# Performance work log

Measured on AMD Instinct MI355X. Metric: run time of the kernel, lower is better.

Reference implementation:

```python
import jax, jax.numpy as jnp
import numpy as np
from jax import lax

N_STEPS = 96
N_MAT = 4
N_STRIKES = 201
PERIOD = N_STEPS // N_MAT  # 24
BATCH = 8192
T_HORIZON = 2.0
RFR = 0.05
S0 = 100.0
DT = T_HORIZON / N_STEPS
SQRT_DT = DT ** 0.5
DF = float(np.exp(-RFR * DT))  # one-step discount factor


def _drift_nets(p, x):
    # x: [3, B]; three stacked MLPs (sigma_S, b_V, sigma_V), n=net axis -> [3, 1, B]
    W0, b0, W1, b1, W2, b2, W3, b3 = p
    h = jax.nn.relu(jnp.einsum('nof,fb->nob', W0, x) + b0[:, :, None])
    h = jax.nn.relu(jnp.einsum('nof,nfb->nob', W1, h) + b1[:, :, None])
    h = jax.nn.relu(jnp.einsum('nof,nfb->nob', W2, h) + b2[:, :, None])
    return jnp.einsum('nof,nfb->nob', W3, h) + b3[:, :, None]


def _hedge_net(p, x):
    # x: [2, B] -> [N_STRIKES*N_MAT, B]
    W0, b0, W1, b1, W2, b2, W3, b3, W4, b4 = p
    h = jax.nn.relu(W0 @ x + b0[:, None])
    h = jax.nn.relu(W1 @ h + b1[:, None])
    h = jax.nn.relu(W2 @ h + b2[:, None])
    h = jax.nn.relu(W3 @ h + b3[:, None])
    return W4 @ h + b4[:, None]


def _forward(nW0, nb0, nW1, nb1, nW2, nb2, nW3, nb3,
             hW0, hb0, hW1, hb1, hW2, hb2, hW3, hb3, hW4, hb4,
             rho, V0, strikes, noise1, noise2, remat=False):
    dtype = noise1.dtype
    B = noise1.shape[1]
    rho_s = rho[0]
    S = jnp.full((B,), S0, dtype)
    V = jnp.ones((B,), dtype) * V0[0]
    H = jnp.zeros((N_STRIKES, N_MAT, B), dtype)  # hedging accumulator
    prices = jnp.zeros((N_STRIKES, N_MAT), dtype)
    variance = jnp.zeros((N_STRIKES, N_MAT), dtype)
    for m in range(N_MAT):  # one MLP set per maturity period (timegridNet idx)
        nP = (nW0[:, m], nb0[:, m], nW1[:, m], nb1[:, m],
              nW2[:, m], nb2[:, m], nW3[:, m], nb3[:, m])
        hP = (hW0[m], hb0[m], hW1[m], hb1[m], hW2[m], hb2[m],
              hW3[m], hb3[m], hW4[m], hb4[m])

        def step(carry, xs, nP=nP, hP=hP):
            S, V, H = carry
            t_i, n1, n2 = xs
            t = t_i * jnp.ones_like(S)
            X = jnp.stack([t, S, V], 0)  # [3, B]
            raw = _drift_nets(nP, X)
            raw_d = _drift_nets(nP, lax.stop_gradient(X))  # X.detach() path
            vals = raw / (1.0 + jnp.abs(raw_d) * SQRT_DT)
            sig_S, b_V, sig_V = vals[0, 0], vals[1, 0], vals[2, 0]
            b_S = S * RFR / (1.0 + jnp.abs(lax.stop_gradient(S) * RFR) * SQRT_DT)
            dW = SQRT_DT * n2
            dB = rho_s * dW + jnp.sqrt(1.0 - rho_s ** 2) * SQRT_DT * n1
            S_new = S + b_S * DT + sig_S * dB
            V_new = jax.nn.relu(V + b_V * DT + sig_V * dW)  # clamp(.., 0)
            hedge = _hedge_net(hP, jnp.stack([t, lax.stop_gradient(S)], 0))
            hedge = hedge.reshape(N_STRIKES, N_MAT, -1)
            H_new = H + DF * lax.stop_gradient(S) * lax.stop_gradient(sig_S) * hedge * dW
            return (S_new, V_new, H_new), None

        if remat:
            step = jax.checkpoint(step)
        ts = (jnp.arange(PERIOD, dtype=dtype) + m * PERIOD) * DT  # (i-1)*dt
        xs = (ts, noise1[m * PERIOD:(m + 1) * PERIOD], noise2[m * PERIOD:(m + 1) * PERIOD])
        (S, V, H), _ = lax.scan(step, (S, V, H), xs)
        disc = DF ** ((m + 1) * PERIOD)
        payoff = disc * jax.nn.relu(S[None, :] - strikes) - H[:, m]  # [201, B]
        prices = prices.at[:, m].set(jnp.mean(payoff, axis=1))
        variance = variance.at[:, m].set(jnp.var(payoff, axis=1, ddof=1))  # torch unbiased var
    return prices, variance


def setup_inputs() -> dict:
    key = jax.random.key(0)
    ks = jax.random.split(key, 24)
    f32 = jnp.float32

    def w(k, shape, fan_in):
        return (jax.random.normal(k, shape, f32) / np.sqrt(fan_in)).astype(f32)

    def b(k, shape):
        return 0.01 * jax.random.normal(k, shape, f32)

    inp = {}
    inp['nW0'] = w(ks[0], (3, 4, 32, 3), 3)
    inp['nb0'] = b(ks[1], (3, 4, 32))
    inp['nW1'] = w(ks[2], (3, 4, 32, 32), 32)
    inp['nb1'] = b(ks[3], (3, 4, 32))
    inp['nW2'] = w(ks[4], (3, 4, 32, 32), 32)
    inp['nb2'] = b(ks[5], (3, 4, 32))
    inp['nW3'] = w(ks[6], (3, 4, 1, 32), 32)
    inp['nb3'] = b(ks[7], (3, 4, 1))
    inp['hW0'] = w(ks[8], (4, 64, 2), 2)
    inp['hb0'] = b(ks[9], (4, 64))
    inp['hW1'] = w(ks[10], (4, 64, 64), 64)
    inp['hb1'] = b(ks[11], (4, 64))
    inp['hW2'] = w(ks[12], (4, 64, 64), 64)
    inp['hb2'] = b(ks[13], (4, 64))
    inp['hW3'] = w(ks[14], (4, 64, 64), 64)
    inp['hb3'] = b(ks[15], (4, 64))
    inp['hW4'] = w(ks[16], (4, 804, 64), 64)
    inp['hb4'] = b(ks[17], (4, 804))
    inp['rho'] = jnp.array([0.3], f32)
    inp['V0'] = jnp.array([0.04], f32)
    inp['strikes'] = jnp.linspace(50.0, 150.0, N_STRIKES, dtype=f32).reshape(-1, 1)
    inp['noise1'] = jax.random.normal(ks[18], (N_STEPS, BATCH), f32)
    inp['noise2'] = jax.random.normal(ks[19], (N_STEPS, BATCH), f32)
    return inp


def reference(nW0, nb0, nW1, nb1, nW2, nb2, nW3, nb3,
              hW0, hb0, hW1, hb1, hW2, hb2, hW3, hb3, hW4, hb4,
              rho, V0, strikes, noise1, noise2):
    return _forward(nW0, nb0, nW1, nb1, nW2, nb2, nW3, nb3,
                    hW0, hb0, hW1, hb1, hW2, hb2, hW3, hb3, hW4, hb4,
                    rho, V0, strikes, noise1, noise2)
```

## Files before the change

### kernel.cpp

```cpp
#include <hip/hip_runtime.h>
#include <math.h>

#define TPB      128
#define NBLOCKS  512
#define PPB      16
#define BATCHN   8192
#define NMAT     4
#define PERS     24
#define NK       201
#define DSTR     124
#define HSTR     76
#define GSTR     68
#define GSC      (1.0f/4096.0f)
#define GUNSC    4096.0f

typedef _Float16 f16;
typedef _Float16 f16x4 __attribute__((ext_vector_type(4)));
typedef _Float16 f16x8 __attribute__((ext_vector_type(8)));
typedef float    f32x4 __attribute__((ext_vector_type(4)));

template<int N> struct IC { static constexpr int v = N; };

#define LDS_FENCE() asm volatile("s_waitcnt lgkmcnt(0)" ::: "memory")

__device__ __forceinline__ f16x8 relu8(f16x8 v){
#pragma unroll
  for (int i = 0; i < 8; ++i) v[i] = (v[i] > (f16)0.f) ? v[i] : (f16)0.f;
  return v;
}
__device__ __forceinline__ f16x8 cvt88(float4 a, float4 b){
  f16x8 r;
  r[0]=(f16)a.x; r[1]=(f16)a.y; r[2]=(f16)a.z; r[3]=(f16)a.w;
  r[4]=(f16)b.x; r[5]=(f16)b.y; r[6]=(f16)b.z; r[7]=(f16)b.w;
  return r;
}
__device__ __forceinline__ f16x4 cvt4(float4 a){
  f16x4 r; r[0]=(f16)a.x; r[1]=(f16)a.y; r[2]=(f16)a.z; r[3]=(f16)a.w; return r;
}

__global__ __launch_bounds__(TPB, 1)
void sde_kernel(const float* __restrict__ nW0, const float* __restrict__ nb0,
                const float* __restrict__ nW1, const float* __restrict__ nb1,
                const float* __restrict__ nW2, const float* __restrict__ nb2,
                const float* __restrict__ nW3, const float* __restrict__ nb3,
                const float* __restrict__ hW0, const float* __restrict__ hb0,
                const float* __restrict__ hW1, const float* __restrict__ hb1,
                const float* __restrict__ hW2, const float* __restrict__ hb2,
                const float* __restrict__ hW3, const float* __restrict__ hb3,
                const float* __restrict__ hW4, const float* __restrict__ hb4,
                const float* __restrict__ rho, const float* __restrict__ V0,
                const float* __restrict__ strikes,
                const float* __restrict__ noise1, const float* __restrict__ noise2,
                float* __restrict__ part1, float* __restrict__ part2)
{
  __shared__ __align__(16) f16   bbD [PPB*DSTR];
  __shared__ __align__(16) f16   bbH1[PPB*HSTR];
  __shared__ __align__(16) f16   bbH2[PPB*HSTR];
  __shared__ __align__(16) float Gsave[NMAT*PPB*GSTR];
  __shared__ float mbS[2][PPB], mbc[2][PPB];
  __shared__ float CstL[NMAT*PPB];
  __shared__ float SfinL[PPB];
  __shared__ float strikesL[NK];

  const int tid  = threadIdx.x;
  const int wv   = tid >> 6;
  const int lane = tid & 63;
  const int L15  = lane & 15;
  const int G    = lane >> 4;
  const int gpath = blockIdx.x * PPB + L15;

  const float DTf = (float)(2.0/96.0);
  const float SDT = 0.14433756729740643f;
  const float DFf = (float)exp(-0.05 * 2.0 / 96.0);
  const float rho_s = rho[0];
  const float rt1m  = sqrtf(1.f - rho_s*rho_s);

  for (int k = tid; k < NK; k += TPB) strikesL[k] = strikes[k];

  float S = 100.f, Vv = V0[0];
  __syncthreads();

  auto maturity = [&](auto MC){
    constexpr int m = decltype(MC)::v;

    f16x8 aD1[6], aD2[6];  f16x4 bD1r[6], bD2r[6];  f32x4 w3r[6];
    f16x8 w0r[3][4];       float b30=0.f, b31=0.f, b32=0.f;
    f16x8 aH[3][4][2];     f16x4 bHr[3][4];         f16x8 wh0r[2][3];
    float Gacc[16];        float Cacc = 0.f;
    float pn1 = 0.f, pn2 = 0.f;

    if (wv == 0){
#pragma unroll
      for (int t6 = 0; t6 < 6; ++t6){
        const int n  = t6 >> 1;
        const int o  = ((t6 & 1) << 4) + L15;
        const int ob = ((t6 & 1) << 4) + 4*G;
        const float* p1 = nW1 + (size_t)(((n*4+m)*32)+o)*32 + G*8;
        aD1[t6] = cvt88(*(const float4*)p1, *(const float4*)(p1+4));
        const float* p2 = nW2 + (size_t)(((n*4+m)*32)+o)*32 + G*8;
        aD2[t6] = cvt88(*(const float4*)p2, *(const float4*)(p2+4));
        bD1r[t6] = cvt4(*(const float4*)(nb1 + (n*4+m)*32 + ob));
        bD2r[t6] = cvt4(*(const float4*)(nb2 + (n*4+m)*32 + ob));
        w3r[t6]  = *(const f32x4*)(nW3 + (n*4+m)*32 + ob);
      }
      b30 = nb3[m]; b31 = nb3[4+m]; b32 = nb3[8+m];
#pragma unroll
      for (int n = 0; n < 3; ++n){
        f16x8 wt, ws, wvv, bz;
#pragma unroll
        for (int j = 0; j < 8; ++j){
          const int o = G*8 + j;
          const float* p = nW0 + (size_t)(((n*4+m)*32)+o)*3;
          wt[j]=(f16)p[0]; ws[j]=(f16)p[1]; wvv[j]=(f16)p[2];
          bz[j]=(f16)nb0[(n*4+m)*32+o];
        }
        w0r[n][0]=wt; w0r[n][1]=ws; w0r[n][2]=wvv; w0r[n][3]=bz;
      }
      pn1 = noise1[(size_t)(m*PERS)*BATCHN + gpath];
      pn2 = noise2[(size_t)(m*PERS)*BATCHN + gpath];
    } else {
#pragma unroll
      for (int L = 0; L < 3; ++L){
        const float* W = (L==0)?hW1:(L==1)?hW2:hW3;
        const float* B = (L==0)?hb1:(L==1)?hb2:hb3;
#pragma unroll
        for (int mt = 0; mt < 4; ++mt){
#pragma unroll
          for (int kt = 0; kt < 2; ++kt){
            const float* src = W + (size_t)m*4096 + (16*mt + L15)*64 + kt*32 + G*8;
            aH[L][mt][kt] = cvt88(*(const float4*)src, *(const float4*)(src+4));
          }
          bHr[L][mt] = cvt4(*(const float4*)(B + m*64 + mt*16 + 4*G));
        }
      }
#pragma unroll
      for (int kt = 0; kt < 2; ++kt){
        f16x8 wt, ws, bz;
#pragma unroll
        for (int j = 0; j < 8; ++j){
          const int o = kt*32 + G*8 + j;
          wt[j]=(f16)hW0[m*128 + o*2];
          ws[j]=(f16)hW0[m*128 + o*2 + 1];
          bz[j]=(f16)hb0[m*64 + o];
        }
        wh0r[kt][0]=wt; wh0r[kt][1]=ws; wh0r[kt][2]=bz;
      }
#pragma unroll
      for (int j = 0; j < 16; ++j) Gacc[j] = 0.f;
    }

#pragma unroll 1
    for (int i = 0; i <= PERS; ++i){
      if (wv == 0){
        if (i < PERS){
          const int gstep = m*PERS + i;
          const float t = (float)gstep * DTf;
          if (lane < PPB) mbS[i & 1][L15] = S;
          float nn1 = 0.f, nn2 = 0.f;
          if (i+1 < PERS){
            nn1 = noise1[(size_t)(gstep+1)*BATCHN + gpath];
            nn2 = noise2[(size_t)(gstep+1)*BATCHN + gpath];
          }
          const f16 th=(f16)t, Sh=(f16)S, Vh=(f16)Vv;
          f16x8 bfr[3];
#pragma unroll
          for (int n = 0; n < 3; ++n)
            bfr[n] = relu8(w0r[n][0]*th + w0r[n][1]*Sh + w0r[n][2]*Vh + w0r[n][3]);
#pragma unroll
          for (int t6 = 0; t6 < 6; ++t6){
            f32x4 acc = {(float)bD1r[t6][0],(float)bD1r[t6][1],(float)bD1r[t6][2],(float)bD1r[t6][3]};
            acc = __builtin_amdgcn_mfma_f32_16x16x32_f16(aD1[t6], bfr[t6>>1], acc, 0,0,0);
            f16x4 o4;
            o4[0]=(f16)fmaxf(acc[0],0.f); o4[1]=(f16)fmaxf(acc[1],0.f);
            o4[2]=(f16)fmaxf(acc[2],0.f); o4[3]=(f16)fmaxf(acc[3],0.f);
            *(f16x4*)&bbD[L15*DSTR + t6*16 + 4*G] = o4;
          }
          LDS_FENCE();
          f16x8 bl[3];
#pragma unroll
          for (int n = 0; n < 3; ++n)
            bl[n] = *(const f16x8*)&bbD[L15*DSTR + n*32 + G*8];
          f32x4 c2[6];
#pragma unroll
          for (int t6 = 0; t6 < 6; ++t6){
            f32x4 acc = {(float)bD2r[t6][0],(float)bD2r[t6][1],(float)bD2r[t6][2],(float)bD2r[t6][3]};
            c2[t6] = __builtin_amdgcn_mfma_f32_16x16x32_f16(aD2[t6], bl[t6>>1], acc, 0,0,0);
          }
          float pr0=0.f, pr1=0.f, pr2=0.f;
#pragma unroll
          for (int t6 = 0; t6 < 6; ++t6){
            const f32x4 w4 = w3r[t6];
            const float pp = w4[0]*fmaxf(c2[t6][0],0.f)+w4[1]*fmaxf(c2[t6][1],0.f)
                           + w4[2]*fmaxf(c2[t6][2],0.f)+w4[3]*fmaxf(c2[t6][3],0.f);
            if (t6<2) pr0+=pp; else if (t6<4) pr1+=pp; else pr2+=pp;
          }
          pr0 += __shfl_xor(pr0,16); pr0 += __shfl_xor(pr0,32);
          pr1 += __shfl_xor(pr1,16); pr1 += __shfl_xor(pr1,32);
          pr2 += __shfl_xor(pr2,16); pr2 += __shfl_xor(pr2,32);
          const float r0=pr0+b30, r1=pr1+b31, r2=pr2+b32;
          const float sigS = r0/(1.f+fabsf(r0)*SDT);
          const float bV   = r1/(1.f+fabsf(r1)*SDT);
          const float sigV = r2/(1.f+fabsf(r2)*SDT);
          const float sr = S*0.05f;
          const float bS = sr/(1.f+fabsf(sr)*SDT);
          const float dW = SDT*pn2;
          const float dB = rho_s*dW + rt1m*SDT*pn1;
          const float c  = DFf*S*sigS*dW;
          Cacc += c;
          if (lane < PPB) mbc[i & 1][L15] = c;
          S  = S + bS*DTf + sigS*dB;
          Vv = fmaxf(Vv + bV*DTf + sigV*dW, 0.f);
          pn1 = nn1; pn2 = nn2;
        }
      } else {
        if (i >= 1){
          const int s = i - 1;
          const float t = (float)(m*PERS + s) * DTf;
          const float Sj = mbS[s & 1][L15];
          const float c  = mbc[s & 1][L15];
          const f16 th=(f16)t, Sh=(f16)Sj;
          f16x8 bh0 = relu8(wh0r[0][0]*th + wh0r[0][1]*Sh + wh0r[0][2]);
          f16x8 bh1 = relu8(wh0r[1][0]*th + wh0r[1][1]*Sh + wh0r[1][2]);
#pragma unroll
          for (int mt = 0; mt < 4; ++mt){
            f32x4 acc = {(float)bHr[0][mt][0],(float)bHr[0][mt][1],(float)bHr[0][mt][2],(float)bHr[0][mt][3]};
            acc = __builtin_amdgcn_mfma_f32_16x16x32_f16(aH[0][mt][0], bh0, acc, 0,0,0);
            acc = __builtin_amdgcn_mfma_f32_16x16x32_f16(aH[0][mt][1], bh1, acc, 0,0,0);
            f16x4 o4;
            o4[0]=(f16)fmaxf(acc[0],0.f); o4[1]=(f16)fmaxf(acc[1],0.f);
            o4[2]=(f16)fmaxf(acc[2],0.f); o4[3]=(f16)fmaxf(acc[3],0.f);
            *(f16x4*)&bbH1[L15*HSTR + mt*16 + 4*G] = o4;
          }
          LDS_FENCE();
          f16x8 x0 = *(const f16x8*)&bbH1[L15*HSTR +      G*8];
          f16x8 x1 = *(const f16x8*)&bbH1[L15*HSTR + 32 + G*8];
#pragma unroll
          for (int mt = 0; mt < 4; ++mt){
            f32x4 acc = {(float)bHr[1][mt][0],(float)bHr[1][mt][1],(float)bHr[1][mt][2],(float)bHr[1][mt][3]};
            acc = __builtin_amdgcn_mfma_f32_16x16x32_f16(aH[1][mt][0], x0, acc, 0,0,0);
            acc = __builtin_amdgcn_mfma_f32_16x16x32_f16(aH[1][mt][1], x1, acc, 0,0,0);
            f16x4 o4;
            o4[0]=(f16)fmaxf(acc[0],0.f); o4[1]=(f16)fmaxf(acc[1],0.f);
            o4[2]=(f16)fmaxf(acc[2],0.f); o4[3]=(f16)fmaxf(acc[3],0.f);
            *(f16x4*)&bbH2[L15*HSTR + mt*16 + 4*G] = o4;
          }
          LDS_FENCE();
          x0 = *(const f16x8*)&bbH2[L15*HSTR +      G*8];
          x1 = *(const f16x8*)&bbH2[L15*HSTR + 32 + G*8];
#pragma unroll
          for (int mt = 0; mt < 4; ++mt){
            f32x4 acc = {(float)bHr[2][mt][0],(float)bHr[2][mt][1],(float)bHr[2][mt][2],(float)bHr[2][mt][3]};
            acc = __builtin_amdgcn_mfma_f32_16x16x32_f16(aH[2][mt][0], x0, acc, 0,0,0);
            acc = __builtin_amdgcn_mfma_f32_16x16x32_f16(aH[2][mt][1], x1, acc, 0,0,0);
            Gacc[mt*4+0] += c*fmaxf(acc[0],0.f);
            Gacc[mt*4+1] += c*fmaxf(acc[1],0.f);
            Gacc[mt*4+2] += c*fmaxf(acc[2],0.f);
            Gacc[mt*4+3] += c*fmaxf(acc[3],0.f);
          }
        }
      }
      __syncthreads();
    }

    if (wv == 0){
      if (lane < PPB){ SfinL[L15] = S; CstL[m*PPB + L15] = Cacc; }
    } else {
#pragma unroll
      for (int mt = 0; mt < 4; ++mt){
        f32x4 gv = {Gacc[mt*4+0], Gacc[mt*4+1], Gacc[mt*4+2], Gacc[mt*4+3]};
        *(f32x4*)&Gsave[(size_t)(m*PPB + L15)*GSTR + mt*16 + 4*G] = gv;
      }
    }
    __syncthreads();

    {
      const float discm = (float)exp(-0.05*(2.0/96.0)*(double)(PERS*(m+1)));
      const float Sfin = SfinL[L15];
      float Cc[m+1];
      f16x8 Bf[m+1][2];
#pragma unroll
      for (int q = 0; q <= m; ++q){
        Cc[q] = CstL[q*PPB + L15];
#pragma unroll
        for (int kt = 0; kt < 2; ++kt){
          const float* gp = &Gsave[(size_t)(q*PPB + L15)*GSTR + kt*32 + G*8];
          const f32x4 g0 = *(const f32x4*)gp;
          const f32x4 g1 = *(const f32x4*)(gp + 4);
          f16x8 b;
          b[0]=(f16)(g0[0]*GSC); b[1]=(f16)(g0[1]*GSC); b[2]=(f16)(g0[2]*GSC); b[3]=(f16)(g0[3]*GSC);
          b[4]=(f16)(g1[0]*GSC); b[5]=(f16)(g1[1]*GSC); b[6]=(f16)(g1[2]*GSC); b[7]=(f16)(g1[3]*GSC);
          Bf[q][kt] = b;
        }
      }
      for (int mt = wv; mt < 13; mt += 2){
        const int ksr = min(16*mt + L15, 200);
        f32x4 acc = {0.f, 0.f, 0.f, 0.f};
#pragma unroll
        for (int q = 0; q <= m; ++q){
#pragma unroll
          for (int kt = 0; kt < 2; ++kt){
            const float* ap = hW4 + (size_t)(q*804 + ksr*4 + m)*64 + kt*32 + G*8;
            const f16x8 a = cvt88(*(const float4*)ap, *(const float4*)(ap+4));
            acc = __builtin_amdgcn_mfma_f32_16x16x32_f16(a, Bf[q][kt], acc, 0,0,0);
          }
        }
#pragma unroll
        for (int r = 0; r < 4; ++r){
          const int k2  = 16*mt + 4*G + r;
          const int k2c = min(k2, 200);
          float ac = acc[r] * GUNSC;
#pragma unroll
          for (int q = 0; q <= m; ++q)
            ac = fmaf(hb4[q*804 + k2c*4 + m], Cc[q], ac);
          const float pay = discm*fmaxf(Sfin - strikesL[k2c], 0.f) - ac;
          float s1 = pay, s2 = pay*pay;
          s1 += __shfl_xor(s1,1); s1 += __shfl_xor(s1,2);
          s1 += __shfl_xor(s1,4); s1 += __shfl_xor(s1,8);
          s2 += __shfl_xor(s2,1); s2 += __shfl_xor(s2,2);
          s2 += __shfl_xor(s2,4); s2 += __shfl_xor(s2,8);
          if (L15 == 0 && k2 < NK){
            part1[(size_t)(m*NK + k2)*NBLOCKS + blockIdx.x] = s1;
            part2[(size_t)(m*NK + k2)*NBLOCKS + blockIdx.x] = s2;
          }
        }
      }
    }
  };

  maturity(IC<0>{});
  maturity(IC<1>{});
  maturity(IC<2>{});
  maturity(IC<3>{});
}

__global__ __launch_bounds__(256)
void finalize_kernel(const float* __restrict__ part1,
                     const float* __restrict__ part2,
                     float* __restrict__ out)
{
  const int j   = blockIdx.x;
  const int m   = j / NK, k = j % NK;
  const int tid = threadIdx.x;
  double s1 = (double)part1[(size_t)j*NBLOCKS + tid]
            + (double)part1[(size_t)j*NBLOCKS + 256 + tid];
  double s2 = (double)part2[(size_t)j*NBLOCKS + tid]
            + (double)part2[(size_t)j*NBLOCKS + 256 + tid];
#pragma unroll
  for (int d = 32; d > 0; d >>= 1){
    s1 += __shfl_down(s1, d, 64);
    s2 += __shfl_down(s2, d, 64);
  }
  __shared__ double r1[4], r2[4];
  if ((tid & 63) == 0){ r1[tid>>6] = s1; r2[tid>>6] = s2; }
  __syncthreads();
  if (tid == 0){
    const double t1 = r1[0]+r1[1]+r1[2]+r1[3];
    const double t2 = r2[0]+r2[1]+r2[2]+r2[3];
    const double mean = t1 / 8192.0;
    const double var  = (t2 - t1*t1/8192.0) / 8191.0;
    out[k*NMAT + m]            = (float)mean;
    out[NK*NMAT + k*NMAT + m]  = (float)var;
  }
}

extern "C" void kernel_launch(void* const* d_in, const int* in_sizes, int n_in,
                              void* d_out, int out_size, void* d_ws, size_t ws_size,
                              hipStream_t stream)
{
  (void)in_sizes; (void)n_in; (void)out_size; (void)ws_size;
  const float* nW0 = (const float*)d_in[0];
  const float* nb0 = (const float*)d_in[1];
  const float* nW1 = (const float*)d_in[2];
  const float* nb1 = (const float*)d_in[3];
  const float* nW2 = (const float*)d_in[4];
  const float* nb2 = (const float*)d_in[5];
  const float* nW3 = (const float*)d_in[6];
  const float* nb3 = (const float*)d_in[7];
  const float* hW0 = (const float*)d_in[8];
  const float* hb0 = (const float*)d_in[9];
  const float* hW1 = (const float*)d_in[10];
  const float* hb1 = (const float*)d_in[11];
  const float* hW2 = (const float*)d_in[12];
  const float* hb2 = (const float*)d_in[13];
  const float* hW3 = (const float*)d_in[14];
  const float* hb3 = (const float*)d_in[15];
  const float* hW4 = (const float*)d_in[16];
  const float* hb4 = (const float*)d_in[17];
  const float* rho = (const float*)d_in[18];
  const float* V0  = (const float*)d_in[19];
  const float* strikes = (const float*)d_in[20];
  const float* noise1  = (const float*)d_in[21];
  const float* noise2  = (const float*)d_in[22];

  float* part1 = (float*)d_ws;
  float* part2 = part1 + (size_t)NMAT*NK*NBLOCKS;

  sde_kernel<<<NBLOCKS, TPB, 0, stream>>>(nW0, nb0, nW1, nb1, nW2, nb2, nW3, nb3,
                                          hW0, hb0, hW1, hb1, hW2, hb2, hW3, hb3,
                                          hW4, hb4, rho, V0, strikes, noise1, noise2,
                                          part1, part2);

  finalize_kernel<<<NMAT*NK, 256, 0, stream>>>(part1, part2, (float*)d_out);
}
```

Before: 309.6 us.

## Split fused SDE kernel into drift scan, batched hedge, and payoff kernels

The single fused kernel ran a drift-network wave and a hedge-network wave in lockstep with block-wide barriers each step. The work is now split into three kernels. A 64-thread drift scan writes per-step S and c values to global memory. A hedge kernel processes all 4 maturities in parallel (4x the blocks) and writes accumulated G values. A separate payoff kernel does the hW4 GEMM and partial sums. This removes the per-step barrier coupling and exposes more parallelism in the hedge stage, at the cost of extra global-memory traffic and kernel launches.

```diff
diff --git a/kernel.cpp b/kernel.cpp
--- a/kernel.cpp
+++ b/kernel.cpp
@@ -1,16 +1,13 @@
 #include <hip/hip_runtime.h>
 #include <math.h>
 
-#define TPB      128
-#define NBLOCKS  512
-#define PPB      16
 #define BATCHN   8192
 #define NMAT     4
 #define PERS     24
 #define NK       201
+#define NPG      512
 #define DSTR     124
 #define HSTR     76
-#define GSTR     68
 #define GSC      (1.0f/4096.0f)
 #define GUNSC    4096.0f
 
@@ -38,36 +35,22 @@
   f16x4 r; r[0]=(f16)a.x; r[1]=(f16)a.y; r[2]=(f16)a.z; r[3]=(f16)a.w; return r;
 }
 
-__global__ __launch_bounds__(TPB, 1)
-void sde_kernel(const float* __restrict__ nW0, const float* __restrict__ nb0,
+__global__ __launch_bounds__(64, 2)
+void drift_scan(const float* __restrict__ nW0, const float* __restrict__ nb0,
                 const float* __restrict__ nW1, const float* __restrict__ nb1,
                 const float* __restrict__ nW2, const float* __restrict__ nb2,
                 const float* __restrict__ nW3, const float* __restrict__ nb3,
-                const float* __restrict__ hW0, const float* __restrict__ hb0,
-                const float* __restrict__ hW1, const float* __restrict__ hb1,
-                const float* __restrict__ hW2, const float* __restrict__ hb2,
-                const float* __restrict__ hW3, const float* __restrict__ hb3,
-                const float* __restrict__ hW4, const float* __restrict__ hb4,
                 const float* __restrict__ rho, const float* __restrict__ V0,
-                const float* __restrict__ strikes,
                 const float* __restrict__ noise1, const float* __restrict__ noise2,
-                float* __restrict__ part1, float* __restrict__ part2)
+                float* __restrict__ Sbuf, float* __restrict__ Cbuf,
+                float* __restrict__ CstB, float* __restrict__ SfinB)
 {
-  __shared__ __align__(16) f16   bbD [PPB*DSTR];
-  __shared__ __align__(16) f16   bbH1[PPB*HSTR];
-  __shared__ __align__(16) f16   bbH2[PPB*HSTR];
-  __shared__ __align__(16) float Gsave[NMAT*PPB*GSTR];
-  __shared__ float mbS[2][PPB], mbc[2][PPB];
-  __shared__ float CstL[NMAT*PPB];
-  __shared__ float SfinL[PPB];
-  __shared__ float strikesL[NK];
-
-  const int tid  = threadIdx.x;
-  const int wv   = tid >> 6;
-  const int lane = tid & 63;
+  __shared__ __align__(16) f16 bbD[16*DSTR];
+
+  const int lane = threadIdx.x;
   const int L15  = lane & 15;
   const int G    = lane >> 4;
-  const int gpath = blockIdx.x * PPB + L15;
+  const int gpath = blockIdx.x * 16 + L15;
 
   const float DTf = (float)(2.0/96.0);
   const float SDT = 0.14433756729740643f;
@@ -75,255 +58,109 @@
   const float rho_s = rho[0];
   const float rt1m  = sqrtf(1.f - rho_s*rho_s);
 
-  for (int k = tid; k < NK; k += TPB) strikesL[k] = strikes[k];
-
   float S = 100.f, Vv = V0[0];
-  __syncthreads();
 
   auto maturity = [&](auto MC){
     constexpr int m = decltype(MC)::v;
 
     f16x8 aD1[6], aD2[6];  f16x4 bD1r[6], bD2r[6];  f32x4 w3r[6];
-    f16x8 w0r[3][4];       float b30=0.f, b31=0.f, b32=0.f;
-    f16x8 aH[3][4][2];     f16x4 bHr[3][4];         f16x8 wh0r[2][3];
-    float Gacc[16];        float Cacc = 0.f;
-    float pn1 = 0.f, pn2 = 0.f;
-
-    if (wv == 0){
+    f16x8 w0r[3][4];
+#pragma unroll
+    for (int t6 = 0; t6 < 6; ++t6){
+      const int n  = t6 >> 1;
+      const int o  = ((t6 & 1) << 4) + L15;
+      const int ob = ((t6 & 1) << 4) + 4*G;
+      const float* p1 = nW1 + (size_t)(((n*4+m)*32)+o)*32 + G*8;
+      aD1[t6] = cvt88(*(const float4*)p1, *(const float4*)(p1+4));
+      const float* p2 = nW2 + (size_t)(((n*4+m)*32)+o)*32 + G*8;
+      aD2[t6] = cvt88(*(const float4*)p2, *(const float4*)(p2+4));
+      bD1r[t6] = cvt4(*(const float4*)(nb1 + (n*4+m)*32 + ob));
+      bD2r[t6] = cvt4(*(const float4*)(nb2 + (n*4+m)*32 + ob));
+      w3r[t6]  = *(const f32x4*)(nW3 + (n*4+m)*32 + ob);
+    }
+    const float b30 = nb3[m], b31 = nb3[4+m], b32 = nb3[8+m];
+#pragma unroll
+    for (int n = 0; n < 3; ++n){
+      f16x8 wt, ws, wvv, bz;
+#pragma unroll
+      for (int j = 0; j < 8; ++j){
+        const int o = G*8 + j;
+        const float* p = nW0 + (size_t)(((n*4+m)*32)+o)*3;
+        wt[j]=(f16)p[0]; ws[j]=(f16)p[1]; wvv[j]=(f16)p[2];
+        bz[j]=(f16)nb0[(n*4+m)*32+o];
+      }
+      w0r[n][0]=wt; w0r[n][1]=ws; w0r[n][2]=wvv; w0r[n][3]=bz;
+    }
+    float pn1 = noise1[(size_t)(m*PERS)*BATCHN + gpath];
+    float pn2 = noise2[(size_t)(m*PERS)*BATCHN + gpath];
+    float Cacc = 0.f;
+
+#pragma unroll 1
+    for (int s = 0; s < PERS; ++s){
+      const int gstep = m*PERS + s;
+      const float t = (float)gstep * DTf;
+      float nn1 = 0.f, nn2 = 0.f;
+      if (s+1 < PERS){
+        nn1 = noise1[(size_t)(gstep+1)*BATCHN + gpath];
+        nn2 = noise2[(size_t)(gstep+1)*BATCHN + gpath];
+      }
+      const f16 th=(f16)t, Sh=(f16)S, Vh=(f16)Vv;
+      f16x8 bfr[3];
+#pragma unroll
+      for (int n = 0; n < 3; ++n)
+        bfr[n] = relu8(w0r[n][0]*th + w0r[n][1]*Sh + w0r[n][2]*Vh + w0r[n][3]);
 #pragma unroll
       for (int t6 = 0; t6 < 6; ++t6){
-        const int n  = t6 >> 1;
-        const int o  = ((t6 & 1) << 4) + L15;
-        const int ob = ((t6 & 1) << 4) + 4*G;
-        const float* p1 = nW1 + (size_t)(((n*4+m)*32)+o)*32 + G*8;
-        aD1[t6] = cvt88(*(const float4*)p1, *(const float4*)(p1+4));
-        const float* p2 = nW2 + (size_t)(((n*4+m)*32)+o)*32 + G*8;
-        aD2[t6] = cvt88(*(const float4*)p2, *(const float4*)(p2+4));
-        bD1r[t6] = cvt4(*(const float4*)(nb1 + (n*4+m)*32 + ob));
-        bD2r[t6] = cvt4(*(const float4*)(nb2 + (n*4+m)*32 + ob));
-        w3r[t6]  = *(const f32x4*)(nW3 + (n*4+m)*32 + ob);
-      }
-      b30 = nb3[m]; b31 = nb3[4+m]; b32 = nb3[8+m];
-#pragma unroll
-      for (int n = 0; n < 3; ++n){
-        f16x8 wt, ws, wvv, bz;
-#pragma unroll
-        for (int j = 0; j < 8; ++j){
-          const int o = G*8 + j;
-          const float* p = nW0 + (size_t)(((n*4+m)*32)+o)*3;
-          wt[j]=(f16)p[0]; ws[j]=(f16)p[1]; wvv[j]=(f16)p[2];
-          bz[j]=(f16)nb0[(n*4+m)*32+o];
-        }
-        w0r[n][0]=wt; w0r[n][1]=ws; w0r[n][2]=wvv; w0r[n][3]=bz;
-      }
-      pn1 = noise1[(size_t)(m*PERS)*BATCHN + gpath];
-      pn2 = noise2[(size_t)(m*PERS)*BATCHN + gpath];
-    } else {
-#pragma unroll
-      for (int L = 0; L < 3; ++L){
-        const float* W = (L==0)?hW1:(L==1)?hW2:hW3;
-        const float* B = (L==0)?hb1:(L==1)?hb2:hb3;
-#pragma unroll
-        for (int mt = 0; mt < 4; ++mt){
-#pragma unroll
-          for (int kt = 0; kt < 2; ++kt){
-            const float* src = W + (size_t)m*4096 + (16*mt + L15)*64 + kt*32 + G*8;
-            aH[L][mt][kt] = cvt88(*(const float4*)src, *(const float4*)(src+4));
-          }
-          bHr[L][mt] = cvt4(*(const float4*)(B + m*64 + mt*16 + 4*G));
-        }
-      }
-#pragma unroll
-      for (int kt = 0; kt < 2; ++kt){
-        f16x8 wt, ws, bz;
-#pragma unroll
-        for (int j = 0; j < 8; ++j){
-          const int o = kt*32 + G*8 + j;
-          wt[j]=(f16)hW0[m*128 + o*2];
-          ws[j]=(f16)hW0[m*128 + o*2 + 1];
-          bz[j]=(f16)hb0[m*64 + o];
-        }
-        wh0r[kt][0]=wt; wh0r[kt][1]=ws; wh0r[kt][2]=bz;
-      }
-#pragma unroll
-      for (int j = 0; j < 16; ++j) Gacc[j] = 0.f;
-    }
-
-#pragma unroll 1
-    for (int i = 0; i <= PERS; ++i){
-      if (wv == 0){
-        if (i < PERS){
-          const int gstep = m*PERS + i;
-          const float t = (float)gstep * DTf;
-          if (lane < PPB) mbS[i & 1][L15] = S;
-          float nn1 = 0.f, nn2 = 0.f;
-          if (i+1 < PERS){
-            nn1 = noise1[(size_t)(gstep+1)*BATCHN + gpath];
-            nn2 = noise2[(size_t)(gstep+1)*BATCHN + gpath];
-          }
-          const f16 th=(f16)t, Sh=(f16)S, Vh=(f16)Vv;
-          f16x8 bfr[3];
-#pragma unroll
-          for (int n = 0; n < 3; ++n)
-            bfr[n] = relu8(w0r[n][0]*th + w0r[n][1]*Sh + w0r[n][2]*Vh + w0r[n][3]);
-#pragma unroll
-          for (int t6 = 0; t6 < 6; ++t6){
-            f32x4 acc = {(float)bD1r[t6][0],(float)bD1r[t6][1],(float)bD1r[t6][2],(float)bD1r[t6][3]};
-            acc = __builtin_amdgcn_mfma_f32_16x16x32_f16(aD1[t6], bfr[t6>>1], acc, 0,0,0);
-            f16x4 o4;
-            o4[0]=(f16)fmaxf(acc[0],0.f); o4[1]=(f16)fmaxf(acc[1],0.f);
-            o4[2]=(f16)fmaxf(acc[2],0.f); o4[3]=(f16)fmaxf(acc[3],0.f);
-            *(f16x4*)&bbD[L15*DSTR + t6*16 + 4*G] = o4;
-          }
-          LDS_FENCE();
-          f16x8 bl[3];
-#pragma unroll
-          for (int n = 0; n < 3; ++n)
-            bl[n] = *(const f16x8*)&bbD[L15*DSTR + n*32 + G*8];
-          f32x4 c2[6];
-#pragma unroll
-          for (int t6 = 0; t6 < 6; ++t6){
-            f32x4 acc = {(float)bD2r[t6][0],(float)bD2r[t6][1],(float)bD2r[t6][2],(float)bD2r[t6][3]};
-            c2[t6] = __builtin_amdgcn_mfma_f32_16x16x32_f16(aD2[t6], bl[t6>>1], acc, 0,0,0);
-          }
-          float pr0=0.f, pr1=0.f, pr2=0.f;
-#pragma unroll
-          for (int t6 = 0; t6 < 6; ++t6){
-            const f32x4 w4 = w3r[t6];
-            const float pp = w4[0]*fmaxf(c2[t6][0],0.f)+w4[1]*fmaxf(c2[t6][1],0.f)
-                           + w4[2]*fmaxf(c2[t6][2],0.f)+w4[3]*fmaxf(c2[t6][3],0.f);
-            if (t6<2) pr0+=pp; else if (t6<4) pr1+=pp; else pr2+=pp;
-          }
-          pr0 += __shfl_xor(pr0,16); pr0 += __shfl_xor(pr0,32);
-          pr1 += __shfl_xor(pr1,16); pr1 += __shfl_xor(pr1,32);
-          pr2 += __shfl_xor(pr2,16); pr2 += __shfl_xor(pr2,32);
-          const float r0=pr0+b30, r1=pr1+b31, r2=pr2+b32;
-          const float sigS = r0/(1.f+fabsf(r0)*SDT);
-          const float bV   = r1/(1.f+fabsf(r1)*SDT);
-          const float sigV = r2/(1.f+fabsf(r2)*SDT);
-          const float sr = S*0.05f;
-          const float bS = sr/(1.f+fabsf(sr)*SDT);
-          const float dW = SDT*pn2;
-          const float dB = rho_s*dW + rt1m*SDT*pn1;
-          const float c  = DFf*S*sigS*dW;
-          Cacc += c;
-          if (lane < PPB) mbc[i & 1][L15] = c;
-          S  = S + bS*DTf + sigS*dB;
-          Vv = fmaxf(Vv + bV*DTf + sigV*dW, 0.f);
-          pn1 = nn1; pn2 = nn2;
-        }
-      } else {
-        if (i >= 1){
-          const int s = i - 1;
-          const float t = (float)(m*PERS + s) * DTf;
-          const float Sj = mbS[s & 1][L15];
-          const float c  = mbc[s & 1][L15];
-          const f16 th=(f16)t, Sh=(f16)Sj;
-          f16x8 bh0 = relu8(wh0r[0][0]*th + wh0r[0][1]*Sh + wh0r[0][2]);
-          f16x8 bh1 = relu8(wh0r[1][0]*th + wh0r[1][1]*Sh + wh0r[1][2]);
-#pragma unroll
-          for (int mt = 0; mt < 4; ++mt){
-            f32x4 acc = {(float)bHr[0][mt][0],(float)bHr[0][mt][1],(float)bHr[0][mt][2],(float)bHr[0][mt][3]};
-            acc = __builtin_amdgcn_mfma_f32_16x16x32_f16(aH[0][mt][0], bh0, acc, 0,0,0);
-            acc = __builtin_amdgcn_mfma_f32_16x16x32_f16(aH[0][mt][1], bh1, acc, 0,0,0);
-            f16x4 o4;
-            o4[0]=(f16)fmaxf(acc[0],0.f); o4[1]=(f16)fmaxf(acc[1],0.f);
-            o4[2]=(f16)fmaxf(acc[2],0.f); o4[3]=(f16)fmaxf(acc[3],0.f);
-            *(f16x4*)&bbH1[L15*HSTR + mt*16 + 4*G] = o4;
-          }
-          LDS_FENCE();
-          f16x8 x0 = *(const f16x8*)&bbH1[L15*HSTR +      G*8];
-          f16x8 x1 = *(const f16x8*)&bbH1[L15*HSTR + 32 + G*8];
-#pragma unroll
-          for (int mt = 0; mt < 4; ++mt){
-            f32x4 acc = {(float)bHr[1][mt][0],(float)bHr[1][mt][1],(float)bHr[1][mt][2],(float)bHr[1][mt][3]};
-            acc = __builtin_amdgcn_mfma_f32_16x16x32_f16(aH[1][mt][0], x0, acc, 0,0,0);
-            acc = __builtin_amdgcn_mfma_f32_16x16x32_f16(aH[1][mt][1], x1, acc, 0,0,0);
-            f16x4 o4;
-            o4[0]=(f16)fmaxf(acc[0],0.f); o4[1]=(f16)fmaxf(acc[1],0.f);
-            o4[2]=(f16)fmaxf(acc[2],0.f); o4[3]=(f16)fmaxf(acc[3],0.f);
-            *(f16x4*)&bbH2[L15*HSTR + mt*16 + 4*G] = o4;
-          }
-          LDS_FENCE();
-          x0 = *(const f16x8*)&bbH2[L15*HSTR +      G*8];
-          x1 = *(const f16x8*)&bbH2[L15*HSTR + 32 + G*8];
-#pragma unroll
-          for (int mt = 0; mt < 4; ++mt){
-            f32x4 acc = {(float)bHr[2][mt][0],(float)bHr[2][mt][1],(float)bHr[2][mt][2],(float)bHr[2][mt][3]};
-            acc = __builtin_amdgcn_mfma_f32_16x16x32_f16(aH[2][mt][0], x0, acc, 0,0,0);
-            acc = __builtin_amdgcn_mfma_f32_16x16x32_f16(aH[2][mt][1], x1, acc, 0,0,0);
-            Gacc[mt*4+0] += c*fmaxf(acc[0],0.f);
-            Gacc[mt*4+1] += c*fmaxf(acc[1],0.f);
-            Gacc[mt*4+2] += c*fmaxf(acc[2],0.f);
-            Gacc[mt*4+3] += c*fmaxf(acc[3],0.f);
-          }
-        }
-      }
-      __syncthreads();
-    }
-
-    if (wv == 0){
-      if (lane < PPB){ SfinL[L15] = S; CstL[m*PPB + L15] = Cacc; }
-    } else {
-#pragma unroll
-      for (int mt = 0; mt < 4; ++mt){
-        f32x4 gv = {Gacc[mt*4+0], Gacc[mt*4+1], Gacc[mt*4+2], Gacc[mt*4+3]};
-        *(f32x4*)&Gsave[(size_t)(m*PPB + L15)*GSTR + mt*16 + 4*G] = gv;
-      }
-    }
-    __syncthreads();
-
-    {
-      const float discm = (float)exp(-0.05*(2.0/96.0)*(double)(PERS*(m+1)));
-      const float Sfin = SfinL[L15];
-      float Cc[m+1];
-      f16x8 Bf[m+1][2];
-#pragma unroll
-      for (int q = 0; q <= m; ++q){
-        Cc[q] = CstL[q*PPB + L15];
-#pragma unroll
-        for (int kt = 0; kt < 2; ++kt){
-          const float* gp = &Gsave[(size_t)(q*PPB + L15)*GSTR + kt*32 + G*8];
-          const f32x4 g0 = *(const f32x4*)gp;
-          const f32x4 g1 = *(const f32x4*)(gp + 4);
-          f16x8 b;
-          b[0]=(f16)(g0[0]*GSC); b[1]=(f16)(g0[1]*GSC); b[2]=(f16)(g0[2]*GSC); b[3]=(f16)(g0[3]*GSC);
-          b[4]=(f16)(g1[0]*GSC); b[5]=(f16)(g1[1]*GSC); b[6]=(f16)(g1[2]*GSC); b[7]=(f16)(g1[3]*GSC);
-          Bf[q][kt] = b;
-        }
-      }
-      for (int mt = wv; mt < 13; mt += 2){
-        const int ksr = min(16*mt + L15, 200);
-        f32x4 acc = {0.f, 0.f, 0.f, 0.f};
-#pragma unroll
-        for (int q = 0; q <= m; ++q){
-#pragma unroll
-          for (int kt = 0; kt < 2; ++kt){
-            const float* ap = hW4 + (size_t)(q*804 + ksr*4 + m)*64 + kt*32 + G*8;
-            const f16x8 a = cvt88(*(const float4*)ap, *(const float4*)(ap+4));
-            acc = __builtin_amdgcn_mfma_f32_16x16x32_f16(a, Bf[q][kt], acc, 0,0,0);
-          }
-        }
-#pragma unroll
-        for (int r = 0; r < 4; ++r){
-          const int k2  = 16*mt + 4*G + r;
-          const int k2c = min(k2, 200);
-          float ac = acc[r] * GUNSC;
-#pragma unroll
-          for (int q = 0; q <= m; ++q)
-            ac = fmaf(hb4[q*804 + k2c*4 + m], Cc[q], ac);
-          const float pay = discm*fmaxf(Sfin - strikesL[k2c], 0.f) - ac;
-          float s1 = pay, s2 = pay*pay;
-          s1 += __shfl_xor(s1,1); s1 += __shfl_xor(s1,2);
-          s1 += __shfl_xor(s1,4); s1 += __shfl_xor(s1,8);
-          s2 += __shfl_xor(s2,1); s2 += __shfl_xor(s2,2);
-          s2 += __shfl_xor(s2,4); s2 += __shfl_xor(s2,8);
-          if (L15 == 0 && k2 < NK){
-            part1[(size_t)(m*NK + k2)*NBLOCKS + blockIdx.x] = s1;
-            part2[(size_t)(m*NK + k2)*NBLOCKS + blockIdx.x] = s2;
-          }
-        }
-      }
+        f32x4 acc = {(float)bD1r[t6][0],(float)bD1r[t6][1],(float)bD1r[t6][2],(float)bD1r[t6][3]};
+        acc = __builtin_amdgcn_mfma_f32_16x16x32_f16(aD1[t6], bfr[t6>>1], acc, 0,0,0);
+        f16x4 o4;
+        o4[0]=(f16)fmaxf(acc[0],0.f); o4[1]=(f16)fmaxf(acc[1],0.f);
+        o4[2]=(f16)fmaxf(acc[2],0.f); o4[3]=(f16)fmaxf(acc[3],0.f);
+        *(f16x4*)&bbD[L15*DSTR + t6*16 + 4*G] = o4;
+      }
+      LDS_FENCE();
+      f16x8 bl[3];
+#pragma unroll
+      for (int n = 0; n < 3; ++n)
+        bl[n] = *(const f16x8*)&bbD[L15*DSTR + n*32 + G*8];
+      f32x4 c2[6];
+#pragma unroll
+      for (int t6 = 0; t6 < 6; ++t6){
+        f32x4 acc = {(float)bD2r[t6][0],(float)bD2r[t6][1],(float)bD2r[t6][2],(float)bD2r[t6][3]};
+        c2[t6] = __builtin_amdgcn_mfma_f32_16x16x32_f16(aD2[t6], bl[t6>>1], acc, 0,0,0);
+      }
+      float pr0=0.f, pr1=0.f, pr2=0.f;
+#pragma unroll
+      for (int t6 = 0; t6 < 6; ++t6){
+        const f32x4 w4 = w3r[t6];
+        const float pp = w4[0]*fmaxf(c2[t6][0],0.f)+w4[1]*fmaxf(c2[t6][1],0.f)
+                       + w4[2]*fmaxf(c2[t6][2],0.f)+w4[3]*fmaxf(c2[t6][3],0.f);
+        if (t6<2) pr0+=pp; else if (t6<4) pr1+=pp; else pr2+=pp;
+      }
+      pr0 += __shfl_xor(pr0,16); pr0 += __shfl_xor(pr0,32);
+      pr1 += __shfl_xor(pr1,16); pr1 += __shfl_xor(pr1,32);
+      pr2 += __shfl_xor(pr2,16); pr2 += __shfl_xor(pr2,32);
+      const float r0=pr0+b30, r1=pr1+b31, r2=pr2+b32;
+      const float sigS = r0/(1.f+fabsf(r0)*SDT);
+      const float bV   = r1/(1.f+fabsf(r1)*SDT);
+      const float sigV = r2/(1.f+fabsf(r2)*SDT);
+      const float sr = S*0.05f;
+      const float bS = sr/(1.f+fabsf(sr)*SDT);
+      const float dW = SDT*pn2;
+      const float dB = rho_s*dW + rt1m*SDT*pn1;
+      const float c  = DFf*S*sigS*dW;
+      Cacc += c;
+      if (G == 0){
+        Sbuf[(size_t)gpath*96 + gstep] = S;
+        Cbuf[(size_t)gpath*96 + gstep] = c;
+      }
+      S  = S + bS*DTf + sigS*dB;
+      Vv = fmaxf(Vv + bV*DTf + sigV*dW, 0.f);
+      pn1 = nn1; pn2 = nn2;
+    }
+    if (G == 0){
+      CstB [m*BATCHN + gpath] = Cacc;
+      SfinB[m*BATCHN + gpath] = S;
     }
   };
 
@@ -331,6 +168,195 @@
   maturity(IC<1>{});
   maturity(IC<2>{});
   maturity(IC<3>{});
+}
+
+__global__ __launch_bounds__(64, 2)
+void hedge_batch(const float* __restrict__ hW0, const float* __restrict__ hb0,
+                 const float* __restrict__ hW1, const float* __restrict__ hb1,
+                 const float* __restrict__ hW2, const float* __restrict__ hb2,
+                 const float* __restrict__ hW3, const float* __restrict__ hb3,
+                 const float* __restrict__ Sbuf, const float* __restrict__ Cbuf,
+                 float* __restrict__ Gbuf)
+{
+  __shared__ __align__(16) f16 bbH1[16*HSTR];
+  __shared__ __align__(16) f16 bbH2[16*HSTR];
+
+  const int m  = blockIdx.x >> 9;
+  const int pg = blockIdx.x & 511;
+  const int lane = threadIdx.x;
+  const int L15  = lane & 15;
+  const int G    = lane >> 4;
+  const int gpath = pg*16 + L15;
+
+  const float DTf = (float)(2.0/96.0);
+
+  f16x8 aH[3][4][2];  f16x4 bHr[3][4];  f16x8 wh0r[2][3];
+#pragma unroll
+  for (int L = 0; L < 3; ++L){
+    const float* W = (L==0)?hW1:(L==1)?hW2:hW3;
+    const float* B = (L==0)?hb1:(L==1)?hb2:hb3;
+#pragma unroll
+    for (int mt = 0; mt < 4; ++mt){
+#pragma unroll
+      for (int kt = 0; kt < 2; ++kt){
+        const float* src = W + (size_t)m*4096 + (16*mt + L15)*64 + kt*32 + G*8;
+        aH[L][mt][kt] = cvt88(*(const float4*)src, *(const float4*)(src+4));
+      }
+      bHr[L][mt] = cvt4(*(const float4*)(B + m*64 + mt*16 + 4*G));
+    }
+  }
+#pragma unroll
+  for (int kt = 0; kt < 2; ++kt){
+    f16x8 wt, ws, bz;
+#pragma unroll
+    for (int j = 0; j < 8; ++j){
+      const int o = kt*32 + G*8 + j;
+      wt[j]=(f16)hW0[m*128 + o*2];
+      ws[j]=(f16)hW0[m*128 + o*2 + 1];
+      bz[j]=(f16)hb0[m*64 + o];
+    }
+    wh0r[kt][0]=wt; wh0r[kt][1]=ws; wh0r[kt][2]=bz;
+  }
+
+  float Gacc[16];
+#pragma unroll
+  for (int j = 0; j < 16; ++j) Gacc[j] = 0.f;
+
+  float pS = Sbuf[(size_t)gpath*96 + m*PERS];
+  float pc = Cbuf[(size_t)gpath*96 + m*PERS];
+
+#pragma unroll 1
+  for (int s = 0; s < PERS; ++s){
+    const float t  = (float)(m*PERS + s) * DTf;
+    const float Sj = pS;
+    const float c  = pc;
+    if (s+1 < PERS){
+      pS = Sbuf[(size_t)gpath*96 + m*PERS + s + 1];
+      pc = Cbuf[(size_t)gpath*96 + m*PERS + s + 1];
+    }
+    const f16 th=(f16)t, Sh=(f16)Sj;
+    f16x8 bh0 = relu8(wh0r[0][0]*th + wh0r[0][1]*Sh + wh0r[0][2]);
+    f16x8 bh1 = relu8(wh0r[1][0]*th + wh0r[1][1]*Sh + wh0r[1][2]);
+#pragma unroll
+    for (int mt = 0; mt < 4; ++mt){
+      f32x4 acc = {(float)bHr[0][mt][0],(float)bHr[0][mt][1],(float)bHr[0][mt][2],(float)bHr[0][mt][3]};
+      acc = __builtin_amdgcn_mfma_f32_16x16x32_f16(aH[0][mt][0], bh0, acc, 0,0,0);
+      acc = __builtin_amdgcn_mfma_f32_16x16x32_f16(aH[0][mt][1], bh1, acc, 0,0,0);
+      f16x4 o4;
+      o4[0]=(f16)fmaxf(acc[0],0.f); o4[1]=(f16)fmaxf(acc[1],0.f);
+      o4[2]=(f16)fmaxf(acc[2],0.f); o4[3]=(f16)fmaxf(acc[3],0.f);
+      *(f16x4*)&bbH1[L15*HSTR + mt*16 + 4*G] = o4;
+    }
+    LDS_FENCE();
+    f16x8 x0 = *(const f16x8*)&bbH1[L15*HSTR +      G*8];
+    f16x8 x1 = *(const f16x8*)&bbH1[L15*HSTR + 32 + G*8];
+#pragma unroll
+    for (int mt = 0; mt < 4; ++mt){
+      f32x4 acc = {(float)bHr[1][mt][0],(float)bHr[1][mt][1],(float)bHr[1][mt][2],(float)bHr[1][mt][3]};
+      acc = __builtin_amdgcn_mfma_f32_16x16x32_f16(aH[1][mt][0], x0, acc, 0,0,0);
+      acc = __builtin_amdgcn_mfma_f32_16x16x32_f16(aH[1][mt][1], x1, acc, 0,0,0);
+      f16x4 o4;
+      o4[0]=(f16)fmaxf(acc[0],0.f); o4[1]=(f16)fmaxf(acc[1],0.f);
+      o4[2]=(f16)fmaxf(acc[2],0.f); o4[3]=(f16)fmaxf(acc[3],0.f);
+      *(f16x4*)&bbH2[L15*HSTR + mt*16 + 4*G] = o4;
+    }
+    LDS_FENCE();
+    x0 = *(const f16x8*)&bbH2[L15*HSTR +      G*8];
+    x1 = *(const f16x8*)&bbH2[L15*HSTR + 32 + G*8];
+#pragma unroll
+    for (int mt = 0; mt < 4; ++mt){
+      f32x4 acc = {(float)bHr[2][mt][0],(float)bHr[2][mt][1],(float)bHr[2][mt][2],(float)bHr[2][mt][3]};
+      acc = __builtin_amdgcn_mfma_f32_16x16x32_f16(aH[2][mt][0], x0, acc, 0,0,0);
+      acc = __builtin_amdgcn_mfma_f32_16x16x32_f16(aH[2][mt][1], x1, acc, 0,0,0);
+      Gacc[mt*4+0] += c*fmaxf(acc[0],0.f);
+      Gacc[mt*4+1] += c*fmaxf(acc[1],0.f);
+      Gacc[mt*4+2] += c*fmaxf(acc[2],0.f);
+      Gacc[mt*4+3] += c*fmaxf(acc[3],0.f);
+    }
+  }
+
+#pragma unroll
+  for (int mt = 0; mt < 4; ++mt)
+#pragma unroll
+    for (int jj = 0; jj < 4; ++jj)
+      Gbuf[((size_t)(m*NPG + pg)*64 + mt*16 + 4*G + jj)*16 + L15] = Gacc[mt*4+jj];
+}
+
+__global__ __launch_bounds__(64, 2)
+void payoff_kernel(const float* __restrict__ hW4, const float* __restrict__ hb4,
+                   const float* __restrict__ strikes,
+                   const float* __restrict__ CstB, const float* __restrict__ SfinB,
+                   const float* __restrict__ Gbuf,
+                   float* __restrict__ part1, float* __restrict__ part2)
+{
+  const int m  = blockIdx.x >> 9;
+  const int pg = blockIdx.x & 511;
+  const int lane = threadIdx.x;
+  const int L15  = lane & 15;
+  const int G    = lane >> 4;
+  const int gpath = pg*16 + L15;
+
+  const float discm = (float)exp(-0.05*(2.0/96.0)*(double)(PERS*(m+1)));
+  const float Sfin  = SfinB[m*BATCHN + gpath];
+
+  float Cc[4];
+  f16x8 Bf[4][2];
+#pragma unroll
+  for (int q = 0; q < 4; ++q){
+    Cc[q] = 0.f;
+    if (q <= m){
+      Cc[q] = CstB[q*BATCHN + gpath];
+#pragma unroll
+      for (int kt = 0; kt < 2; ++kt){
+        f16x8 b;
+#pragma unroll
+        for (int j = 0; j < 8; ++j){
+          const float g = Gbuf[((size_t)(q*NPG + pg)*64 + kt*32 + G*8 + j)*16 + L15];
+          b[j] = (f16)(g * GSC);
+        }
+        Bf[q][kt] = b;
+      }
+    } else {
+      f16x8 z = {};
+      Bf[q][0] = z; Bf[q][1] = z;
+    }
+  }
+
+#pragma unroll 1
+  for (int mt = 0; mt < 13; ++mt){
+    const int ksr = min(16*mt + L15, 200);
+    f32x4 acc = {0.f, 0.f, 0.f, 0.f};
+#pragma unroll
+    for (int q = 0; q < 4; ++q){
+      if (q <= m){
+#pragma unroll
+        for (int kt = 0; kt < 2; ++kt){
+          const float* ap = hW4 + (size_t)(q*804 + ksr*4 + m)*64 + kt*32 + G*8;
+          const f16x8 a = cvt88(*(const float4*)ap, *(const float4*)(ap+4));
+          acc = __builtin_amdgcn_mfma_f32_16x16x32_f16(a, Bf[q][kt], acc, 0,0,0);
+        }
+      }
+    }
+#pragma unroll
+    for (int r = 0; r < 4; ++r){
+      const int k2  = 16*mt + 4*G + r;
+      const int k2c = min(k2, 200);
+      float ac = acc[r] * GUNSC;
+#pragma unroll
+      for (int q = 0; q < 4; ++q)
+        if (q <= m) ac = fmaf(hb4[q*804 + k2c*4 + m], Cc[q], ac);
+      const float pay = discm*fmaxf(Sfin - strikes[k2c], 0.f) - ac;
+      float s1 = pay, s2 = pay*pay;
+      s1 += __shfl_xor(s1,1); s1 += __shfl_xor(s1,2);
+      s1 += __shfl_xor(s1,4); s1 += __shfl_xor(s1,8);
+      s2 += __shfl_xor(s2,1); s2 += __shfl_xor(s2,2);
+      s2 += __shfl_xor(s2,4); s2 += __shfl_xor(s2,8);
+      if (L15 == 0 && k2 < NK){
+        part1[(size_t)(m*NK + k2)*NPG + pg] = s1;
+        part2[(size_t)(m*NK + k2)*NPG + pg] = s2;
+      }
+    }
+  }
 }
 
 __global__ __launch_bounds__(256)
@@ -341,10 +367,10 @@
   const int j   = blockIdx.x;
   const int m   = j / NK, k = j % NK;
   const int tid = threadIdx.x;
-  double s1 = (double)part1[(size_t)j*NBLOCKS + tid]
-            + (double)part1[(size_t)j*NBLOCKS + 256 + tid];
-  double s2 = (double)part2[(size_t)j*NBLOCKS + tid]
-            + (double)part2[(size_t)j*NBLOCKS + 256 + tid];
+  double s1 = (double)part1[(size_t)j*NPG + tid]
+            + (double)part1[(size_t)j*NPG + 256 + tid];
+  double s2 = (double)part2[(size_t)j*NPG + tid]
+            + (double)part2[(size_t)j*NPG + 256 + tid];
 #pragma unroll
   for (int d = 32; d > 0; d >>= 1){
     s1 += __shfl_down(s1, d, 64);
@@ -392,13 +418,23 @@
   const float* noise1  = (const float*)d_in[21];
   const float* noise2  = (const float*)d_in[22];
 
-  float* part1 = (float*)d_ws;
-  float* part2 = part1 + (size_t)NMAT*NK*NBLOCKS;
-
-  sde_kernel<<<NBLOCKS, TPB, 0, stream>>>(nW0, nb0, nW1, nb1, nW2, nb2, nW3, nb3,
-                                          hW0, hb0, hW1, hb1, hW2, hb2, hW3, hb3,
-                                          hW4, hb4, rho, V0, strikes, noise1, noise2,
-                                          part1, part2);
+  float* Sbuf  = (float*)d_ws;
+  float* Cbuf  = Sbuf  + (size_t)BATCHN*96;
+  float* CstB  = Cbuf  + (size_t)BATCHN*96;
+  float* SfinB = CstB  + (size_t)NMAT*BATCHN;
+  float* Gbuf  = SfinB + (size_t)NMAT*BATCHN;
+  float* part1 = Gbuf  + (size_t)NMAT*NPG*64*16;
+  float* part2 = part1 + (size_t)NMAT*NK*NPG;
+
+  drift_scan<<<NPG, 64, 0, stream>>>(nW0, nb0, nW1, nb1, nW2, nb2, nW3, nb3,
+                                     rho, V0, noise1, noise2,
+                                     Sbuf, Cbuf, CstB, SfinB);
+
+  hedge_batch<<<NMAT*NPG, 64, 0, stream>>>(hW0, hb0, hW1, hb1, hW2, hb2, hW3, hb3,
+                                           Sbuf, Cbuf, Gbuf);
+
+  payoff_kernel<<<NMAT*NPG, 64, 0, stream>>>(hW4, hb4, strikes, CstB, SfinB, Gbuf,
+                                             part1, part2);
 
   finalize_kernel<<<NMAT*NK, 256, 0, stream>>>(part1, part2, (float*)d_out);
 }
```

New measurement: 316.7 us. +2.3%, slower.
